# Kernel optimization log

Hardware: AMD Instinct MI355X
Metric: run time of the kernel (lower is better)

Reference implementation:

```python
import jax, jax.numpy as jnp
import numpy as np

B = 16384   # batch of feature vectors
D = 1024    # backbone.hidden_dim
T = 20      # n_tasks
C = 100     # num_classes // n_tasks = n_classes_per_head


def setup_inputs() -> dict:
    key = jax.random.key(0)
    k1, k2, k3, k4 = jax.random.split(key, 4)
    x = jax.random.normal(k1, (B, D), dtype=jnp.float32)
    t = jax.random.randint(k2, (B,), 0, T)  # per-sample task id in [0, T)
    # Stacked per-task Linear params (PyTorch Linear: y = x @ W.T + b, W is [C, D])
    W = jax.random.normal(k3, (T, C, D), dtype=jnp.float32) * (1.0 / np.sqrt(D))
    b = jax.random.normal(k4, (T, C), dtype=jnp.float32) * 0.01
    return {"x": x, "t": t, "W": W, "b": b}


def reference(x, t, W, b):
    """Faithful vectorization of forward_head.

    Original: for each unique task, gather rows with t==task, apply that
    task's Linear, scatter results back into pred. Equivalent math:
    pred[i] = W[t[i]] @ x[i] + b[t[i]].

    We compute all T heads in one dense einsum ([B,T,C] = 131MB, cheap vs a
    [B,C,D] gathered-weight tensor) and select each sample's own task row.
    """
    logits_all = jnp.einsum('bd,tcd->btc', x, W) + b[None, :, :]  # [B, T, C]
    pred = jnp.take_along_axis(logits_all, t[:, None, None], axis=1)[:, 0, :]  # [B, C]
    return pred
```

## Files before the change

kernel.cpp:

```cpp
#include <hip/hip_runtime.h>
#include <hip/hip_bf16.h>

#define NB 16384
#define ND 1024
#define NT 20
#define NC 100
#define NTILES_MAX 280
#define SPLITK 2
#define STEPS 8
#define ABUF 16384
#define BBUF 14336
#define BUFB (ABUF + BBUF)

typedef __bf16  bf16x8 __attribute__((ext_vector_type(8)));
typedef float   f32x4  __attribute__((ext_vector_type(4)));
typedef unsigned short ushort_t;

__device__ __forceinline__ unsigned int f2bf(float f) {
    unsigned int u = __builtin_bit_cast(unsigned int, f);
    u += 0x7FFFu + ((u >> 16) & 1u);
    return u >> 16;
}
__device__ __forceinline__ unsigned long long pack4(float a, float b, float c, float d) {
    return (unsigned long long)f2bf(a)
         | ((unsigned long long)f2bf(b) << 16)
         | ((unsigned long long)f2bf(c) << 32)
         | ((unsigned long long)f2bf(d) << 48);
}
__device__ __forceinline__ bf16x8 mk_frag(float4 a, float4 b) {
    union { unsigned long long u[2]; bf16x8 v; } r;
    r.u[0] = pack4(a.x, a.y, a.z, a.w);
    r.u[1] = pack4(b.x, b.y, b.z, b.w);
    return r.v;
}

__device__ __forceinline__ void async_cp16(const void* g, void* l) {
    auto gp = reinterpret_cast<const __attribute__((address_space(1))) unsigned int*>(
        reinterpret_cast<unsigned long long>(g));
    auto lp = reinterpret_cast<__attribute__((address_space(3))) unsigned int*>(
        static_cast<unsigned int>(reinterpret_cast<unsigned long long>(l)));
    __builtin_amdgcn_global_load_lds(gp, lp, 16, 0, 0);
}


__global__ __launch_bounds__(1024) void prep_kernel(
    const float* __restrict__ W, ushort_t* __restrict__ Wf,
    const int* __restrict__ t, int* __restrict__ offsets,
    int* __restrict__ tiles, int* __restrict__ idx_list)
{
    const int tid = threadIdx.x;
    if (blockIdx.x < 280) {
        int g = blockIdx.x * 1024 + tid;
        int kg   = g & 127;
        int rest = g >> 7;
        int c    = rest % 112;
        int task = rest / 112;
        unsigned long long u0 = 0, u1 = 0;
        if (c < NC) {
            const float* p = W + ((size_t)(task * NC + c)) * ND + kg * 8;
            float4 a = *(const float4*)p;
            float4 b = *(const float4*)(p + 4);
            u0 = pack4(a.x, a.y, a.z, a.w);
            u1 = pack4(b.x, b.y, b.z, b.w);
        }
        size_t dst = (((size_t)task * 32 + (kg >> 2)) * 7 + (c >> 4)) * 512
                   + (size_t)((c & 15) | ((kg & 3) << 4)) * 8;
        *(unsigned long long*)(Wf + dst)     = u0;
        *(unsigned long long*)(Wf + dst + 4) = u1;
        return;
    }
    __shared__ int h[NT], off[NT + 1], cur[NT], tb[NT + 1];
    if (tid < NT) h[tid] = 0;
    __syncthreads();
    const int4* t4 = (const int4*)t;
    int4 v[4];
#pragma unroll
    for (int k = 0; k < 4; ++k) v[k] = t4[tid + k * 1024];
#pragma unroll
    for (int k = 0; k < 4; ++k) {
        atomicAdd(&h[v[k].x], 1); atomicAdd(&h[v[k].y], 1);
        atomicAdd(&h[v[k].z], 1); atomicAdd(&h[v[k].w], 1);
    }
    __syncthreads();
    if (tid == 0) {
        int acc = 0, tv = 0;
        for (int i = 0; i < NT; ++i) {
            off[i] = acc; cur[i] = acc; tb[i] = tv;
            acc += h[i]; tv += (h[i] + 63) >> 6;
        }
        off[NT] = acc; tb[NT] = tv;
    }
    __syncthreads();
    if (tid <= NT) offsets[tid] = off[tid];
    const int ntiles = tb[NT];
    if (tid < NTILES_MAX) {
        int e = -1;
        if (tid < ntiles) {
            int task = 0;
            while (tb[task + 1] <= tid) ++task;
            e = (task << 16) | (tid - tb[task]);
        }
        tiles[tid] = e;
    }
#pragma unroll
    for (int k = 0; k < 4; ++k) {
        int base = (tid + k * 1024) * 4;
        idx_list[atomicAdd(&cur[v[k].x], 1)] = base;
        idx_list[atomicAdd(&cur[v[k].y], 1)] = base + 1;
        idx_list[atomicAdd(&cur[v[k].z], 1)] = base + 2;
        idx_list[atomicAdd(&cur[v[k].w], 1)] = base + 3;
    }
}


__global__ __launch_bounds__(256, 2) void gemm_kernel(
    const float* __restrict__ x, const ushort_t* __restrict__ Wfrag,
    const int* __restrict__ offsets, const int* __restrict__ tiles,
    const int* __restrict__ idx_list, float* __restrict__ out0,
    float* __restrict__ out1)
{
    __shared__ __align__(16) char lds[2 * BUFB];
    const int ent = tiles[blockIdx.x >> 1];
    if (ent < 0) return;
    const int kq   = blockIdx.x & 1;
    const int task = ent >> 16;
    const int m0   = (ent & 0xffff) << 6;
    const int seg  = offsets[task];
    const int cnt  = offsets[task + 1] - seg;

    const int tid  = threadIdx.x;
    const int wid  = tid >> 6;
    const int lane = tid & 63;
    const int csel = lane & 15;
    const int q    = lane >> 4;

    const float* srcA[4];
#pragma unroll
    for (int jj = 0; jj < 4; ++jj) {
        int row  = wid * 16 + jj * 4 + q;
        int logb = (csel * 16) ^ ((row & 7) << 4);
        int sr   = m0 + row; if (sr > cnt - 1) sr = cnt - 1;
        srcA[jj] = x + (size_t)idx_list[seg + sr] * ND + kq * 512 + (logb >> 2);
    }
    const ushort_t* srcB = Wfrag + ((size_t)(task * 32 + kq * 16) * 7) * 512 + lane * 8;
    int bii[4];
#pragma unroll
    for (int jj = 0; jj < 4; ++jj) {
        int i = wid + 4 * jj;
        bii[jj] = (i < 14) ? i : (i - 14);
    }

    auto STAGE = [&](int s, char* Ab) {
        char* Bb = Ab + ABUF;
#pragma unroll
        for (int jj = 0; jj < 4; ++jj)
            async_cp16(srcA[jj] + s * 64, Ab + (wid * 4 + jj) * 1024);
#pragma unroll
        for (int jj = 0; jj < 4; ++jj)
            async_cp16(srcB + (size_t)(s * 14 + bii[jj]) * 512, Bb + bii[jj] * 1024);
    };

    f32x4 acc[7] = {};
    const int rowA = wid * 16 + csel;
    const unsigned swzA = (unsigned)((rowA & 7) << 4);

    auto COMPUTE = [&](const char* Ab) {
        const char* Bb = Ab + ABUF;
        const char* Ar = Ab + rowA * 256;
#pragma unroll
        for (int kkb = 0; kkb < 2; ++kkb) {
            unsigned abase = (unsigned)(kkb * 128 + q * 32);
            float4 a0 = *(const float4*)(Ar + (abase ^ swzA));
            float4 a1 = *(const float4*)(Ar + ((abase + 16) ^ swzA));
            bf16x8 af = mk_frag(a0, a1);
#pragma unroll
            for (int f = 0; f < 7; ++f) {
                bf16x8 bf = *(const bf16x8*)(Bb + (kkb * 7 + f) * 1024 + lane * 16);
                acc[f] = __builtin_amdgcn_mfma_f32_16x16x32_bf16(af, bf, acc[f], 0, 0, 0);
            }
        }
    };

    STAGE(0, lds);
    STAGE(1, lds + BUFB);
    asm volatile("s_waitcnt vmcnt(8)" ::: "memory");
    __builtin_amdgcn_sched_barrier(0);
    __builtin_amdgcn_s_barrier();

#pragma unroll 1
    for (int s = 0; s < STEPS; ++s) {
        char* Ab = lds + (s & 1) * BUFB;
        COMPUTE(Ab);
        if (s == STEPS - 1) break;
        asm volatile("s_waitcnt lgkmcnt(0)" ::: "memory");
        __builtin_amdgcn_s_barrier();
        if (s < STEPS - 2) {
            STAGE(s + 2, Ab);
            asm volatile("s_waitcnt vmcnt(8)" ::: "memory");
        } else {
            asm volatile("s_waitcnt vmcnt(0)" ::: "memory");
        }
        __builtin_amdgcn_sched_barrier(0);
        __builtin_amdgcn_s_barrier();
    }

    float* __restrict__ outP = kq ? out1 : out0;
    int oi[4];
#pragma unroll
    for (int rr = 0; rr < 4; ++rr) {
        int gm = m0 + wid * 16 + q * 4 + rr;
        oi[rr] = (gm < cnt) ? idx_list[seg + gm] : -1;
    }
#pragma unroll
    for (int f = 0; f < 7; ++f) {
        int cg = f * 16 + csel;
        if (cg < NC) {
#pragma unroll
            for (int rr = 0; rr < 4; ++rr)
                if (oi[rr] >= 0)
                    outP[(size_t)oi[rr] * NC + cg] = acc[f][rr];
        }
    }
}


__global__ void finalize_kernel(float* __restrict__ o0, const float* __restrict__ o1,
                                const int* __restrict__ t, const float* __restrict__ bias) {
    int id = blockIdx.x * 256 + threadIdx.x;
    float2 v0 = ((const float2*)o0)[id];
    float2 v1 = ((const float2*)o1)[id];
    int e0 = 2 * id;
    int oi = e0 / NC;
    int c  = e0 - oi * NC;
    const float* brow = bias + t[oi] * NC;
    float2 o;
    o.x = v0.x + v1.x + brow[c];
    o.y = v0.y + v1.y + brow[c + 1];
    ((float2*)o0)[id] = o;
}


extern "C" void kernel_launch(void* const* d_in, const int* in_sizes, int n_in,
                              void* d_out, int out_size, void* d_ws, size_t ws_size,
                              hipStream_t stream) {
    const float* x    = (const float*)d_in[0];
    const int*   t    = (const int*)d_in[1];
    const float* W    = (const float*)d_in[2];
    const float* bias = (const float*)d_in[3];

    char* ws = (char*)d_ws;
    int* offsets  = (int*)ws;
    int* tiles    = (int*)(ws + 128);
    int* idx_list = (int*)(ws + 4352);
    ushort_t* Wf  = (ushort_t*)(ws + 69888);
    float* out1   = (float*)(ws + 4657408);

    prep_kernel    <<<281, 1024, 0, stream>>>(W, Wf, t, offsets, tiles, idx_list);
    gemm_kernel    <<<NTILES_MAX * SPLITK, 256, 0, stream>>>(x, Wf, offsets, tiles,
                                                             idx_list, (float*)d_out,
                                                             out1);
    finalize_kernel<<<NB * NC / 512, 256, 0, stream>>>((float*)d_out, out1, t, bias);
}
```

Measured before the change: 44.58 us.

## Stage A via registers with bf16 conversion before LDS write, raise occupancy

Activation rows are now loaded into registers, converted to bf16 once, and written into a half-size swizzled LDS buffer, instead of being copied as fp32 straight into LDS and converted on every MFMA fragment read. The smaller LDS footprint allows launch bounds to request three workgroups per CU, the main loop is fully unrolled, and output row indices are hoisted to the kernel start. This trades the asynchronous global-to-LDS path for A for register staging with extra vmcnt/lgkmcnt waits, which raises register pressure and could limit the occupancy gain.

Measured after the change: 40.30 us. 9.6% less time.

```diff
diff --git a/kernel.cpp b/kernel.cpp
--- a/kernel.cpp
+++ b/kernel.cpp
@@ -8,7 +8,7 @@
 #define NTILES_MAX 280
 #define SPLITK 2
 #define STEPS 8
-#define ABUF 16384
+#define ABUF 8192
 #define BBUF 14336
 #define BUFB (ABUF + BBUF)
 
@@ -26,12 +26,6 @@
          | ((unsigned long long)f2bf(b) << 16)
          | ((unsigned long long)f2bf(c) << 32)
          | ((unsigned long long)f2bf(d) << 48);
-}
-__device__ __forceinline__ bf16x8 mk_frag(float4 a, float4 b) {
-    union { unsigned long long u[2]; bf16x8 v; } r;
-    r.u[0] = pack4(a.x, a.y, a.z, a.w);
-    r.u[1] = pack4(b.x, b.y, b.z, b.w);
-    return r.v;
 }
 
 __device__ __forceinline__ void async_cp16(const void* g, void* l) {
@@ -113,7 +107,7 @@
 }
 
 
-__global__ __launch_bounds__(256, 2) void gemm_kernel(
+__global__ __launch_bounds__(256, 3) void gemm_kernel(
     const float* __restrict__ x, const ushort_t* __restrict__ Wfrag,
     const int* __restrict__ offsets, const int* __restrict__ tiles,
     const int* __restrict__ idx_list, float* __restrict__ out0,
@@ -134,13 +128,19 @@
     const int csel = lane & 15;
     const int q    = lane >> 4;
 
+    int oi[4];
+#pragma unroll
+    for (int rr = 0; rr < 4; ++rr) {
+        int gm = m0 + wid * 16 + q * 4 + rr;
+        oi[rr] = (gm < cnt) ? idx_list[seg + gm] : -1;
+    }
+
     const float* srcA[4];
 #pragma unroll
     for (int jj = 0; jj < 4; ++jj) {
-        int row  = wid * 16 + jj * 4 + q;
-        int logb = (csel * 16) ^ ((row & 7) << 4);
-        int sr   = m0 + row; if (sr > cnt - 1) sr = cnt - 1;
-        srcA[jj] = x + (size_t)idx_list[seg + sr] * ND + kq * 512 + (logb >> 2);
+        int row = wid * 16 + jj * 4 + q;
+        int sr  = m0 + row; if (sr > cnt - 1) sr = cnt - 1;
+        srcA[jj] = x + (size_t)idx_list[seg + sr] * ND + kq * 512 + csel * 4;
     }
     const ushort_t* srcB = Wfrag + ((size_t)(task * 32 + kq * 16) * 7) * 512 + lane * 8;
     int bii[4];
@@ -150,67 +150,81 @@
         bii[jj] = (i < 14) ? i : (i - 14);
     }
 
-    auto STAGE = [&](int s, char* Ab) {
-        char* Bb = Ab + ABUF;
+    float4 aR[2][4];
+    auto ISSUE_A = [&](int s, int set) {
 #pragma unroll
         for (int jj = 0; jj < 4; ++jj)
-            async_cp16(srcA[jj] + s * 64, Ab + (wid * 4 + jj) * 1024);
+            aR[set][jj] = *(const float4*)(srcA[jj] + s * 64);
+    };
+    auto ISSUE_B = [&](int s, char* Bl) {
 #pragma unroll
         for (int jj = 0; jj < 4; ++jj)
-            async_cp16(srcB + (size_t)(s * 14 + bii[jj]) * 512, Bb + bii[jj] * 1024);
+            async_cp16(srcB + (size_t)(s * 14 + bii[jj]) * 512, Bl + bii[jj] * 1024);
+    };
+    auto WRITE_A = [&](int set, char* Al) {
+#pragma unroll
+        for (int jj = 0; jj < 4; ++jj) {
+            int r = wid * 16 + jj * 4 + q;
+            unsigned off = (unsigned)(r * 128 + ((csel * 8) ^ ((r & 7) << 4)));
+            float4 v = aR[set][jj];
+            *(unsigned long long*)(Al + off) = pack4(v.x, v.y, v.z, v.w);
+        }
     };
 
     f32x4 acc[7] = {};
     const int rowA = wid * 16 + csel;
     const unsigned swzA = (unsigned)((rowA & 7) << 4);
 
-    auto COMPUTE = [&](const char* Ab) {
-        const char* Bb = Ab + ABUF;
-        const char* Ar = Ab + rowA * 256;
+    auto COMPUTE = [&](const char* buf) {
+        const char* Ar = buf + rowA * 128;
+        const char* Bl = buf + ABUF;
 #pragma unroll
         for (int kkb = 0; kkb < 2; ++kkb) {
-            unsigned abase = (unsigned)(kkb * 128 + q * 32);
-            float4 a0 = *(const float4*)(Ar + (abase ^ swzA));
-            float4 a1 = *(const float4*)(Ar + ((abase + 16) ^ swzA));
-            bf16x8 af = mk_frag(a0, a1);
+            bf16x8 af = *(const bf16x8*)(Ar + (((unsigned)(kkb * 64 + q * 16)) ^ swzA));
 #pragma unroll
             for (int f = 0; f < 7; ++f) {
-                bf16x8 bf = *(const bf16x8*)(Bb + (kkb * 7 + f) * 1024 + lane * 16);
+                bf16x8 bf = *(const bf16x8*)(Bl + (kkb * 7 + f) * 1024 + lane * 16);
                 acc[f] = __builtin_amdgcn_mfma_f32_16x16x32_bf16(af, bf, acc[f], 0, 0, 0);
             }
         }
     };
 
-    STAGE(0, lds);
-    STAGE(1, lds + BUFB);
+    char* buf0 = lds;
+    char* buf1 = lds + BUFB;
+
+    ISSUE_A(0, 0); ISSUE_B(0, buf0 + ABUF);
+    ISSUE_A(1, 1); ISSUE_B(1, buf1 + ABUF);
+    asm volatile("s_waitcnt vmcnt(12)" ::: "memory");
+    __builtin_amdgcn_sched_barrier(0);
+    WRITE_A(0, buf0);
     asm volatile("s_waitcnt vmcnt(8)" ::: "memory");
     __builtin_amdgcn_sched_barrier(0);
+    asm volatile("s_waitcnt lgkmcnt(0)" ::: "memory");
     __builtin_amdgcn_s_barrier();
 
-#pragma unroll 1
+#pragma unroll
     for (int s = 0; s < STEPS; ++s) {
-        char* Ab = lds + (s & 1) * BUFB;
-        COMPUTE(Ab);
+        COMPUTE((s & 1) ? buf1 : buf0);
         if (s == STEPS - 1) break;
         asm volatile("s_waitcnt lgkmcnt(0)" ::: "memory");
+        __builtin_amdgcn_sched_barrier(0);
         __builtin_amdgcn_s_barrier();
+        asm volatile("s_waitcnt vmcnt(4)" ::: "memory");
+        __builtin_amdgcn_sched_barrier(0);
+        WRITE_A((s + 1) & 1, (s & 1) ? buf0 : buf1);
         if (s < STEPS - 2) {
-            STAGE(s + 2, Ab);
+            ISSUE_A(s + 2, s & 1);
+            ISSUE_B(s + 2, ((s & 1) ? buf1 : buf0) + ABUF);
             asm volatile("s_waitcnt vmcnt(8)" ::: "memory");
         } else {
             asm volatile("s_waitcnt vmcnt(0)" ::: "memory");
         }
         __builtin_amdgcn_sched_barrier(0);
+        asm volatile("s_waitcnt lgkmcnt(0)" ::: "memory");
         __builtin_amdgcn_s_barrier();
     }
 
     float* __restrict__ outP = kq ? out1 : out0;
-    int oi[4];
-#pragma unroll
-    for (int rr = 0; rr < 4; ++rr) {
-        int gm = m0 + wid * 16 + q * 4 + rr;
-        oi[rr] = (gm < cnt) ? idx_list[seg + gm] : -1;
-    }
 #pragma unroll
     for (int f = 0; f < 7; ++f) {
         int cg = f * 16 + csel;
```
